# Kernel tuning notes

Hardware: AMD Instinct MI355X
Metric: run time of the kernel (lower is better)

The kernel has to match this reference:

```python
import jax, jax.numpy as jnp
import numpy as np

N_HEAD = 16
INPUT_DIM = 1024
D_K = 64


def setup_inputs() -> dict:
    key = jax.random.key(0)
    k1, k2, k3 = jax.random.split(key, 3)
    x = jax.random.normal(k1, (4, 2048, INPUT_DIM), dtype=jnp.float32)
    # xavier_uniform for linear weights
    def xavier(k, shape):
        fan_out, fan_in = shape
        limit = (6.0 / (fan_in + fan_out)) ** 0.5
        return jax.random.uniform(k, shape, jnp.float32, -limit, limit)
    W_qkv = xavier(k2, (3 * D_K * N_HEAD, INPUT_DIM))
    b_qkv = jnp.zeros((3 * D_K * N_HEAD,), jnp.float32)
    W_o = xavier(k3, (D_K * N_HEAD, D_K * N_HEAD))
    b_o = jnp.zeros((D_K * N_HEAD,), jnp.float32)
    return {"x": x, "W_qkv": W_qkv, "b_qkv": b_qkv, "W_o": W_o, "b_o": b_o}


def reference(x, W_qkv, b_qkv, W_o, b_o):
    B, S, _ = x.shape
    h = x @ W_qkv.T + b_qkv                      # (B, S, 3*d_k*H)
    # NOTE: original module reshapes directly (no transpose) to (B, H, S, 3*d_k)
    h = h.reshape(B, N_HEAD, S, 3 * D_K)
    q, k, v = jnp.split(h, 3, axis=-1)           # each (B, H, S, d_k)
    scores = jnp.einsum("bhqd,bhkd->bhqk", q, k) / jnp.sqrt(jnp.float32(D_K))
    attn = jax.nn.softmax(scores, axis=-1)       # (B, H, S, S)
    o = jnp.einsum("bhqk,bhkd->bhqd", attn, v)   # (B, H, S, d_k)
    o = o.transpose(0, 2, 1, 3).reshape(B, S, N_HEAD * D_K)
    return o @ W_o.T + b_o
```

## Files before the change

kernel.cpp:

```cpp
#include <hip/hip_runtime.h>
#include <stdint.h>


typedef __attribute__((ext_vector_type(8))) short short8;
typedef __attribute__((ext_vector_type(4))) short short4v;
typedef __attribute__((ext_vector_type(4))) float f32x4;
typedef __attribute__((ext_vector_type(16))) float f32x16;

#define B_SZ 4
#define S_SZ 2048
#define H_N 16
#define DK 64
#define IN_DIM 1024
#define QKV_DIM 3072
#define MODEL 1024
#define M_ROWS (B_SZ * S_SZ)

#define QSCALE 0.1803368801f

#if __has_builtin(__builtin_amdgcn_exp2f)
#define EXP2(x) __builtin_amdgcn_exp2f(x)
#else
#define EXP2(x) exp2f(x)
#endif

__device__ __forceinline__ short f2bf(float f) {
    union { float f; uint32_t u; } v; v.f = f;
    uint32_t r = v.u + 0x7FFFu + ((v.u >> 16) & 1u);
    return (short)(r >> 16);
}

__device__ __forceinline__ uint32_t pk2f(float a, float b) {
    uint32_t r;
    asm("v_cvt_pk_bf16_f32 %0, %1, %2" : "=v"(r) : "v"(a), "v"(b));
    return r;
}

__device__ __forceinline__ void gld_lds16(const void* g, void* l) {
    __builtin_amdgcn_global_load_lds(
        (const __attribute__((address_space(1))) void*)g,
        (__attribute__((address_space(3))) void*)l, 16, 0, 0);
}

__global__ __launch_bounds__(256) void cvt_kernel(
    const float* __restrict__ x, const float* __restrict__ wq,
    const float* __restrict__ wo, short* __restrict__ xb,
    short* __restrict__ wqb, short* __restrict__ wob) {
    const int NX = M_ROWS * IN_DIM / 4;
    const int NQ = QKV_DIM * IN_DIM / 4;
    const int NO = MODEL * IN_DIM / 4;
    const int total = NX + NQ + NO;
    for (int i = blockIdx.x * blockDim.x + threadIdx.x; i < total;
         i += gridDim.x * blockDim.x) {
        const f32x4* src; short4v* dst; int j;
        if (i < NX)           { src = (const f32x4*)x;  dst = (short4v*)xb;  j = i; }
        else if (i < NX + NQ) { src = (const f32x4*)wq; dst = (short4v*)wqb; j = i - NX; }
        else                  { src = (const f32x4*)wo; dst = (short4v*)wob; j = i - NX - NQ; }
        f32x4 v = src[j];
        short4v o;
        o[0] = f2bf(v[0]); o[1] = f2bf(v[1]); o[2] = f2bf(v[2]); o[3] = f2bf(v[3]);
        dst[j] = o;
    }
}

template <int MODE>
__global__ __launch_bounds__(256, 2) void gemm_bt(
    const short* __restrict__ A, const short* __restrict__ Bm,
    const float* __restrict__ bias, float* __restrict__ Cout,
    short* __restrict__ Qb, short* __restrict__ Kb, short* __restrict__ Vt,
    int M, int N, int K) {
    __shared__ short As[2][128 * 64];
    __shared__ short Bs[2][128 * 64];
    const int tid = threadIdx.x;
    const int wave = tid >> 6, lane = tid & 63;
    const int row16 = lane & 15, kgrp = lane >> 4;
    const int wm = (wave >> 1) * 64, wn = (wave & 1) * 64;
    const int nwg = gridDim.x * gridDim.y;
    const int id = blockIdx.y * gridDim.x + blockIdx.x;
    const int nid = (id & 7) * (nwg >> 3) + (id >> 3);
    const int bn = nid % gridDim.x, bm = nid / gridDim.x;
    const short* Ab = A + (size_t)bm * 128 * K;
    const short* Bb = Bm + (size_t)bn * 128 * K;
    f32x4 acc[4][4] = {};

    const int soff = ((lane & 7) ^ (lane >> 3)) * 8;
#define GSTAGE(BUF, K0)                                                        \
    {                                                                          \
        _Pragma("unroll") for (int l = 0; l < 4; ++l) {                        \
            int r = wave * 8 + (lane >> 3) + l * 32;                           \
            gld_lds16(Ab + (size_t)r * K + (K0) + soff,                        \
                      &As[BUF][(wave * 8 + l * 32) * 64]);                     \
            gld_lds16(Bb + (size_t)r * K + (K0) + soff,                        \
                      &Bs[BUF][(wave * 8 + l * 32) * 64]);                     \
        }                                                                      \
    }

    GSTAGE(0, 0);
    const int NK = K >> 6;
    for (int t = 0; t < NK; ++t) {
        __syncthreads();
        const int cur = t & 1;
        if (t + 1 < NK) GSTAGE(cur ^ 1, (t + 1) * 64);
#pragma unroll
        for (int kk = 0; kk < 2; ++kk) {
            short8 af[4], bfr[4];
#pragma unroll
            for (int i = 0; i < 4; ++i) {
                int R = wm + i * 16 + row16;
                int ch = (kk * 4 + kgrp) ^ (R & 7);
                af[i] = *(const short8*)&As[cur][R * 64 + ch * 8];
            }
#pragma unroll
            for (int j = 0; j < 4; ++j) {
                int R = wn + j * 16 + row16;
                int ch = (kk * 4 + kgrp) ^ (R & 7);
                bfr[j] = *(const short8*)&Bs[cur][R * 64 + ch * 8];
            }
            __builtin_amdgcn_s_setprio(1);
#pragma unroll
            for (int i = 0; i < 4; ++i)
#pragma unroll
                for (int j = 0; j < 4; ++j)
                    acc[i][j] = __builtin_amdgcn_mfma_f32_16x16x32_bf16(
                        af[i], bfr[j], acc[i][j], 0, 0, 0);
            __builtin_amdgcn_s_setprio(0);
        }
    }
#undef GSTAGE
#pragma unroll
    for (int j = 0; j < 4; ++j) {
        int gcol = bn * 128 + wn + j * 16 + row16;
        float bv = bias[gcol];
#pragma unroll
        for (int i = 0; i < 4; ++i) {
#pragma unroll
            for (int r = 0; r < 4; ++r) {
                int grow = bm * 128 + wm + i * 16 + kgrp * 4 + r;
                float val = acc[i][j][r] + bv;
                if (MODE == 1) {
                    Cout[(size_t)grow * N + gcol] = val;
                } else {
                    int b = grow >> 11, so = grow & 2047;
                    int hh = so >> 7, a = so & 127;
                    int rr = gcol / 192, cc = gcol - rr * 192;
                    int ss = a * 16 + rr;
                    int bh = b * H_N + hh;
                    if (cc < 64) {
                        Qb[(((size_t)bh) * S_SZ + ss) * DK + cc] = f2bf(val * QSCALE);
                    } else if (cc < 128) {
                        Kb[(((size_t)bh) * S_SZ + ss) * DK + cc - 64] = f2bf(val);
                    } else {
                        Vt[((size_t)bh * DK + (cc - 128)) * S_SZ + ss] = f2bf(val);
                    }
                }
            }
        }
    }
}

__global__ __launch_bounds__(256, 3) void attn_kernel(
    const short* __restrict__ Qg, const short* __restrict__ Kg,
    const short* __restrict__ Vtg, short* __restrict__ O) {
    __shared__ short Ks[2][64 * 64];
    __shared__ short Vs[2][64 * 64];
    const int tid = threadIdx.x;
    const int wave = tid >> 6, lane = tid & 63;
    const int q = lane & 31, hi = lane >> 5;
    const int id = blockIdx.x;
    const int bh = (id & 7) * 8 + ((id >> 3) & 7);
    const int qt = id >> 6;
    const int b = bh >> 4, h = bh & 15;
    const short* Qp = Qg + (size_t)bh * S_SZ * DK;
    const short* Kp = Kg + (size_t)bh * S_SZ * DK;
    const short* Vp = Vtg + (size_t)bh * DK * S_SZ;
    const int q0 = qt * 128 + wave * 32;

    short8 qf[4];
#pragma unroll
    for (int c = 0; c < 4; ++c)
        qf[c] = *(const short8*)&Qp[(size_t)(q0 + q) * DK + c * 16 + hi * 8];

    f32x16 ot0 = {}, ot1 = {};
    float m_run = -1e30f, l_run = 0.f;

    const int srow0 = wave * 16 + (lane >> 3);
    const int srow1 = srow0 + 8;
    const int sc0 = ((lane & 7) ^ (srow0 & 7)) * 8;
    const int sc1 = ((lane & 7) ^ (srow1 & 7)) * 8;
    const short* kg0 = Kp + (size_t)srow0 * DK + sc0;
    const short* kg1 = Kp + (size_t)srow1 * DK + sc1;
    const short* vg0 = Vp + (size_t)srow0 * S_SZ + sc0;
    const short* vg1 = Vp + (size_t)srow1 * S_SZ + sc1;
#define STAGE(BUF)                                                              \
    {                                                                           \
        gld_lds16(kg0, &Ks[BUF][(wave * 16) * 64]);                             \
        gld_lds16(kg1, &Ks[BUF][(wave * 16 + 8) * 64]);                         \
        gld_lds16(vg0, &Vs[BUF][(wave * 16) * 64]);                             \
        gld_lds16(vg1, &Vs[BUF][(wave * 16 + 8) * 64]);                         \
        kg0 += 64 * DK; kg1 += 64 * DK; vg0 += 64; vg1 += 64;                   \
    }

    STAGE(0);

    const int NT = S_SZ / 64;
    for (int t = 0; t < NT; ++t) {
        __syncthreads();
        const int cur = t & 1;
        if (t + 1 < NT) STAGE(cur ^ 1);

        const int qx = (q & 7) << 3;
        f32x16 st0 = {}, st1 = {};
        __builtin_amdgcn_s_setprio(1);
#pragma unroll
        for (int c = 0; c < 4; ++c) {
            const int sw = (((c * 2 + hi) << 3) ^ qx);
            short8 kf0 = *(const short8*)&Ks[cur][q * 64 + sw];
            short8 kf1 = *(const short8*)&Ks[cur][(32 + q) * 64 + sw];
            st0 = __builtin_amdgcn_mfma_f32_32x32x16_bf16(kf0, qf[c], st0, 0, 0, 0);
            st1 = __builtin_amdgcn_mfma_f32_32x32x16_bf16(kf1, qf[c], st1, 0, 0, 0);
        }
        __builtin_amdgcn_s_setprio(0);

        float ma = fmaxf(fmaxf(st0[0], st0[1]), st0[2]);
        float mb = fmaxf(fmaxf(st0[8], st0[9]), st0[10]);
        float mc = fmaxf(fmaxf(st1[0], st1[1]), st1[2]);
        float md = fmaxf(fmaxf(st1[8], st1[9]), st1[10]);
        ma = fmaxf(fmaxf(ma, st0[3]), st0[4]);
        mb = fmaxf(fmaxf(mb, st0[11]), st0[12]);
        mc = fmaxf(fmaxf(mc, st1[3]), st1[4]);
        md = fmaxf(fmaxf(md, st1[11]), st1[12]);
        ma = fmaxf(fmaxf(ma, st0[5]), st0[6]);
        mb = fmaxf(fmaxf(mb, st0[13]), st0[14]);
        mc = fmaxf(fmaxf(mc, st1[5]), st1[6]);
        md = fmaxf(fmaxf(md, st1[13]), st1[14]);
        ma = fmaxf(ma, st0[7]);
        mb = fmaxf(mb, st0[15]);
        mc = fmaxf(mc, st1[7]);
        md = fmaxf(md, st1[15]);
        float pm = fmaxf(fmaxf(ma, mb), fmaxf(mc, md));
        pm = fmaxf(pm, __shfl_xor(pm, 32));
        if (__any(pm > m_run + 8.f)) {
            float mnew = fmaxf(m_run, pm);
            float corr = EXP2(m_run - mnew);
            m_run = mnew;
            l_run *= corr;
#pragma unroll
            for (int r = 0; r < 16; ++r) { ot0[r] *= corr; ot1[r] *= corr; }
        }
        float s0 = 0.f, s1 = 0.f, s2 = 0.f, s3 = 0.f;
#pragma unroll
        for (int r = 0; r < 16; r += 4) {
            st0[r] = EXP2(st0[r] - m_run);         s0 += st0[r];
            st0[r + 1] = EXP2(st0[r + 1] - m_run); s1 += st0[r + 1];
            st0[r + 2] = EXP2(st0[r + 2] - m_run); s2 += st0[r + 2];
            st0[r + 3] = EXP2(st0[r + 3] - m_run); s3 += st0[r + 3];
        }
#pragma unroll
        for (int r = 0; r < 16; r += 4) {
            st1[r] = EXP2(st1[r] - m_run);         s0 += st1[r];
            st1[r + 1] = EXP2(st1[r + 1] - m_run); s1 += st1[r + 1];
            st1[r + 2] = EXP2(st1[r + 2] - m_run); s2 += st1[r + 2];
            st1[r + 3] = EXP2(st1[r + 3] - m_run); s3 += st1[r + 3];
        }
        float ssum = (s0 + s1) + (s2 + s3);
        ssum += __shfl_xor(ssum, 32);
        l_run += ssum;

        __builtin_amdgcn_s_setprio(1);
#if __has_builtin(__builtin_amdgcn_permlane32_swap)
#define PVCHUNK(ST, B0, CH)                                                    \
    {                                                                          \
        uint32_t A01 = pk2f(ST[(B0) + 0], ST[(B0) + 1]);                       \
        uint32_t A23 = pk2f(ST[(B0) + 2], ST[(B0) + 3]);                       \
        uint32_t B45 = pk2f(ST[(B0) + 4], ST[(B0) + 5]);                       \
        uint32_t B67 = pk2f(ST[(B0) + 6], ST[(B0) + 7]);                       \
        auto sw0 = __builtin_amdgcn_permlane32_swap(A01, B45, false, false);   \
        auto sw1 = __builtin_amdgcn_permlane32_swap(A23, B67, false, false);   \
        union { uint32_t u[4]; short8 s8; } pbu;                               \
        pbu.u[0] = sw0[0]; pbu.u[1] = sw1[0];                                  \
        pbu.u[2] = sw0[1]; pbu.u[3] = sw1[1];                                  \
        const int vsw = ((((CH) * 2 + hi) << 3) ^ qx);                         \
        short8 vf0 = *(const short8*)&Vs[cur][q * 64 + vsw];                   \
        short8 vf1 = *(const short8*)&Vs[cur][(32 + q) * 64 + vsw];            \
        ot0 = __builtin_amdgcn_mfma_f32_32x32x16_bf16(vf0, pbu.s8, ot0, 0, 0, 0); \
        ot1 = __builtin_amdgcn_mfma_f32_32x32x16_bf16(vf1, pbu.s8, ot1, 0, 0, 0); \
    }
#else
#define PVCHUNK(ST, B0, CH)                                                    \
    {                                                                          \
        uint32_t A01 = pk2f(ST[(B0) + 0], ST[(B0) + 1]);                       \
        uint32_t A23 = pk2f(ST[(B0) + 2], ST[(B0) + 3]);                       \
        uint32_t B45 = pk2f(ST[(B0) + 4], ST[(B0) + 5]);                       \
        uint32_t B67 = pk2f(ST[(B0) + 6], ST[(B0) + 7]);                       \
        uint32_t t0 = hi ? A01 : B45, t1 = hi ? A23 : B67;                     \
        uint32_t r0 = (uint32_t)__shfl_xor((int)t0, 32);                       \
        uint32_t r1 = (uint32_t)__shfl_xor((int)t1, 32);                       \
        union { uint32_t u[4]; short8 s8; } pbu;                               \
        pbu.u[0] = hi ? r0 : A01; pbu.u[1] = hi ? r1 : A23;                    \
        pbu.u[2] = hi ? B45 : r0; pbu.u[3] = hi ? B67 : r1;                    \
        const int vsw = ((((CH) * 2 + hi) << 3) ^ qx);                         \
        short8 vf0 = *(const short8*)&Vs[cur][q * 64 + vsw];                   \
        short8 vf1 = *(const short8*)&Vs[cur][(32 + q) * 64 + vsw];            \
        ot0 = __builtin_amdgcn_mfma_f32_32x32x16_bf16(vf0, pbu.s8, ot0, 0, 0, 0); \
        ot1 = __builtin_amdgcn_mfma_f32_32x32x16_bf16(vf1, pbu.s8, ot1, 0, 0, 0); \
    }
#endif
        PVCHUNK(st0, 0, 0);
        PVCHUNK(st0, 8, 1);
        PVCHUNK(st1, 0, 2);
        PVCHUNK(st1, 8, 3);
#undef PVCHUNK
        __builtin_amdgcn_s_setprio(0);
    }
#undef STAGE

    float inv = 1.f / l_run;
    size_t rowbase = ((size_t)b * S_SZ + (q0 + q)) * MODEL + h * DK;
#pragma unroll
    for (int i = 0; i < 4; ++i) {
        short4v v0, v1;
#pragma unroll
        for (int jj = 0; jj < 4; ++jj) {
            v0[jj] = f2bf(ot0[4 * i + jj] * inv);
            v1[jj] = f2bf(ot1[4 * i + jj] * inv);
        }
        *(short4v*)&O[rowbase + 8 * i + 4 * hi] = v0;
        *(short4v*)&O[rowbase + 32 + 8 * i + 4 * hi] = v1;
    }
}

extern "C" void kernel_launch(void* const* d_in, const int* in_sizes, int n_in,
                              void* d_out, int out_size, void* d_ws, size_t ws_size,
                              hipStream_t stream) {
    const float* x    = (const float*)d_in[0];
    const float* Wqkv = (const float*)d_in[1];
    const float* bqkv = (const float*)d_in[2];
    const float* Wo   = (const float*)d_in[3];
    const float* bo   = (const float*)d_in[4];
    float* out = (float*)d_out;
    char* ws = (char*)d_ws;

    short* xb  = (short*)(ws + 0);
    short* wqb = (short*)(ws + 16777216);
    short* wob = (short*)(ws + 23068672);
    short* Qb  = (short*)(ws + 25165824);
    short* Kb  = (short*)(ws + 41943040);
    short* Vt  = (short*)(ws + 58720256);
    short* Ob  = (short*)(ws + 0);

    cvt_kernel<<<dim3(2048), dim3(256), 0, stream>>>(x, Wqkv, Wo, xb, wqb, wob);
    gemm_bt<0><<<dim3(QKV_DIM / 128, M_ROWS / 128), dim3(256), 0, stream>>>(
        xb, wqb, bqkv, nullptr, Qb, Kb, Vt, M_ROWS, QKV_DIM, IN_DIM);
    attn_kernel<<<dim3(1024), dim3(256), 0, stream>>>(Qb, Kb, Vt, Ob);
    gemm_bt<1><<<dim3(MODEL / 128, M_ROWS / 128), dim3(256), 0, stream>>>(
        Ob, wob, bo, out, nullptr, nullptr, nullptr, M_ROWS, MODEL, IN_DIM);
}
```

Before: 225.1 us.

## Reshape GEMM tiles to 256x64 with one wave per row strip and lighter syncs

```diff
diff --git a/kernel.cpp b/kernel.cpp
--- a/kernel.cpp
+++ b/kernel.cpp
@@ -69,73 +69,82 @@
     const float* __restrict__ bias, float* __restrict__ Cout,
     short* __restrict__ Qb, short* __restrict__ Kb, short* __restrict__ Vt,
     int M, int N, int K) {
-    __shared__ short As[2][128 * 64];
-    __shared__ short Bs[2][128 * 64];
+    __shared__ short As[2][256 * 64];
+    __shared__ short Bs[2][64 * 64];
     const int tid = threadIdx.x;
     const int wave = tid >> 6, lane = tid & 63;
     const int row16 = lane & 15, kgrp = lane >> 4;
-    const int wm = (wave >> 1) * 64, wn = (wave & 1) * 64;
+    const int wm = wave * 64;
     const int nwg = gridDim.x * gridDim.y;
     const int id = blockIdx.y * gridDim.x + blockIdx.x;
     const int nid = (id & 7) * (nwg >> 3) + (id >> 3);
     const int bn = nid % gridDim.x, bm = nid / gridDim.x;
-    const short* Ab = A + (size_t)bm * 128 * K;
-    const short* Bb = Bm + (size_t)bn * 128 * K;
+    const short* Ab = A + (size_t)bm * 256 * K;
+    const short* Bb = Bm + (size_t)bn * 64 * K;
     f32x4 acc[4][4] = {};
 
     const int soff = ((lane & 7) ^ (lane >> 3)) * 8;
+    const int arow = wave * 64 + (lane >> 3);
+    const int brow = wave * 16 + (lane >> 3);
 #define GSTAGE(BUF, K0)                                                        \
     {                                                                          \
-        _Pragma("unroll") for (int l = 0; l < 4; ++l) {                        \
-            int r = wave * 8 + (lane >> 3) + l * 32;                           \
-            gld_lds16(Ab + (size_t)r * K + (K0) + soff,                        \
-                      &As[BUF][(wave * 8 + l * 32) * 64]);                     \
-            gld_lds16(Bb + (size_t)r * K + (K0) + soff,                        \
-                      &Bs[BUF][(wave * 8 + l * 32) * 64]);                     \
-        }                                                                      \
-    }
-
+        _Pragma("unroll") for (int l = 0; l < 8; ++l)                          \
+            gld_lds16(Ab + (size_t)(arow + l * 8) * K + (K0) + soff,           \
+                      &As[BUF][(wave * 64 + l * 8) * 64]);                     \
+        _Pragma("unroll") for (int l = 0; l < 2; ++l)                          \
+            gld_lds16(Bb + (size_t)(brow + l * 8) * K + (K0) + soff,           \
+                      &Bs[BUF][(wave * 16 + l * 8) * 64]);                     \
+    }
+
+    const int NK = K >> 6;
     GSTAGE(0, 0);
-    const int NK = K >> 6;
     for (int t = 0; t < NK; ++t) {
-        __syncthreads();
         const int cur = t & 1;
-        if (t + 1 < NK) GSTAGE(cur ^ 1, (t + 1) * 64);
-#pragma unroll
-        for (int kk = 0; kk < 2; ++kk) {
-            short8 af[4], bfr[4];
-#pragma unroll
-            for (int i = 0; i < 4; ++i) {
-                int R = wm + i * 16 + row16;
-                int ch = (kk * 4 + kgrp) ^ (R & 7);
-                af[i] = *(const short8*)&As[cur][R * 64 + ch * 8];
+        __builtin_amdgcn_s_barrier();
+        if (t + 1 < NK) {
+            GSTAGE(cur ^ 1, (t + 1) * 64);
+            asm volatile("s_waitcnt vmcnt(10)" ::: "memory");
+        } else {
+            asm volatile("s_waitcnt vmcnt(0)" ::: "memory");
+        }
+        __builtin_amdgcn_sched_barrier(0);
+        short8 bf[4][2];
+#pragma unroll
+        for (int j = 0; j < 4; ++j) {
+            int R = j * 16 + row16;
+#pragma unroll
+            for (int kk = 0; kk < 2; ++kk)
+                bf[j][kk] = *(const short8*)
+                    &Bs[cur][R * 64 + (((kk * 4 + kgrp) ^ (R & 7)) * 8)];
+        }
+#pragma unroll
+        for (int i = 0; i < 4; ++i) {
+            int R = wm + i * 16 + row16;
+            short8 af0 = *(const short8*)
+                &As[cur][R * 64 + (((kgrp) ^ (R & 7)) * 8)];
+            short8 af1 = *(const short8*)
+                &As[cur][R * 64 + (((4 + kgrp) ^ (R & 7)) * 8)];
+            __builtin_amdgcn_s_setprio(1);
+#pragma unroll
+            for (int j = 0; j < 4; ++j) {
+                acc[i][j] = __builtin_amdgcn_mfma_f32_16x16x32_bf16(
+                    af0, bf[j][0], acc[i][j], 0, 0, 0);
+                acc[i][j] = __builtin_amdgcn_mfma_f32_16x16x32_bf16(
+                    af1, bf[j][1], acc[i][j], 0, 0, 0);
             }
-#pragma unroll
-            for (int j = 0; j < 4; ++j) {
-                int R = wn + j * 16 + row16;
-                int ch = (kk * 4 + kgrp) ^ (R & 7);
-                bfr[j] = *(const short8*)&Bs[cur][R * 64 + ch * 8];
-            }
-            __builtin_amdgcn_s_setprio(1);
-#pragma unroll
-            for (int i = 0; i < 4; ++i)
-#pragma unroll
-                for (int j = 0; j < 4; ++j)
-                    acc[i][j] = __builtin_amdgcn_mfma_f32_16x16x32_bf16(
-                        af[i], bfr[j], acc[i][j], 0, 0, 0);
             __builtin_amdgcn_s_setprio(0);
         }
     }
 #undef GSTAGE
 #pragma unroll
     for (int j = 0; j < 4; ++j) {
-        int gcol = bn * 128 + wn + j * 16 + row16;
+        int gcol = bn * 64 + j * 16 + row16;
         float bv = bias[gcol];
 #pragma unroll
         for (int i = 0; i < 4; ++i) {
 #pragma unroll
             for (int r = 0; r < 4; ++r) {
-                int grow = bm * 128 + wm + i * 16 + kgrp * 4 + r;
+                int grow = bm * 256 + wm + i * 16 + kgrp * 4 + r;
                 float val = acc[i][j][r] + bv;
                 if (MODE == 1) {
                     Cout[(size_t)grow * N + gcol] = val;
@@ -349,9 +358,9 @@
     short* Ob  = (short*)(ws + 0);
 
     cvt_kernel<<<dim3(2048), dim3(256), 0, stream>>>(x, Wqkv, Wo, xb, wqb, wob);
-    gemm_bt<0><<<dim3(QKV_DIM / 128, M_ROWS / 128), dim3(256), 0, stream>>>(
+    gemm_bt<0><<<dim3(QKV_DIM / 64, M_ROWS / 256), dim3(256), 0, stream>>>(
         xb, wqb, bqkv, nullptr, Qb, Kb, Vt, M_ROWS, QKV_DIM, IN_DIM);
     attn_kernel<<<dim3(1024), dim3(256), 0, stream>>>(Qb, Kb, Vt, Ob);
-    gemm_bt<1><<<dim3(MODEL / 128, M_ROWS / 128), dim3(256), 0, stream>>>(
+    gemm_bt<1><<<dim3(MODEL / 64, M_ROWS / 256), dim3(256), 0, stream>>>(
         Ob, wob, bo, out, nullptr, nullptr, nullptr, M_ROWS, MODEL, IN_DIM);
 }
```

Result: slower. 242.5 us (+7.8%).
